# Kernel optimization log

Hardware: AMD Instinct MI355X
Metric: run time of the kernel (lower is better)

## Reference

```python
import jax, jax.numpy as jnp
import numpy as np

B, T, N = 8, 168, 1024
FD, FS, FF = 16, 32, 8
DL, DG, HE, E = 128, 128, 4, 16384
BN = B * N


def _lstm_last(x, Wih, Whh, bih, bhh):
    # x: (BN, T, FD); PyTorch gate order i, f, g, o
    h0 = jnp.zeros((x.shape[0], Whh.shape[1]), x.dtype)
    def step(carry, xt):
        h, c = carry
        g = xt @ Wih.T + h @ Whh.T + bih + bhh
        i, f, gg, o = jnp.split(g, 4, axis=-1)
        c = jax.nn.sigmoid(f) * c + jax.nn.sigmoid(i) * jnp.tanh(gg)
        h = jax.nn.sigmoid(o) * jnp.tanh(c)
        return (h, c), None
    (h, _), _ = jax.lax.scan(step, (h0, h0), jnp.swapaxes(x, 0, 1))
    return h


def _ln(x, g, b):
    mu = x.mean(-1, keepdims=True)
    v = ((x - mu) ** 2).mean(-1, keepdims=True)
    return (x - mu) / jnp.sqrt(v + 1e-5) * g + b


def _gat(x, src, dst, ea, W, a_src, a_dst, a_edge, We, bias):
    # PyG GATConv: concat=False (mean over heads), edge_dim=1, LeakyReLU(0.2)
    xl = (x @ W.T).reshape(BN, HE, -1)                 # (BN, H, C)
    as_ = jnp.sum(xl * a_src, -1)                      # (BN, H)
    ad_ = jnp.sum(xl * a_dst, -1)
    ep = (ea @ We.T).reshape(-1, HE, xl.shape[-1])     # (Eb, H, C)
    ae_ = jnp.sum(ep * a_edge, -1)                     # (Eb, H)
    alpha = jax.nn.leaky_relu(as_[src] + ad_[dst] + ae_, 0.2)
    amax = jax.ops.segment_max(alpha, dst, num_segments=BN)
    ex = jnp.exp(alpha - amax[dst])
    den = jax.ops.segment_sum(ex, dst, num_segments=BN)
    w = ex / den[dst]                                  # softmax over incoming edges
    out = jax.ops.segment_sum(w[:, :, None] * xl[src], dst, num_segments=BN)
    return out.mean(axis=1) + bias


def _forward(fl, edge_index):
    (dyn, fcst, sta, ew,
     lWih, lWhh, lbih, lbhh, sW, sb, fW, fb, uW, ub,
     g0W, g0as, g0ad, g0ae, g0We, g0b,
     g1W, g1as, g1ad, g1ae, g1We, g1b,
     n0g, n0b, n1g, n1b, oW, ob) = fl
    x = jnp.transpose(dyn, (0, 2, 1, 3)).reshape(BN, T, FD)
    z = _lstm_last(x, lWih, lWhh, lbih, lbhh)
    s = jax.nn.relu(sta.reshape(BN, -1) @ sW.T + sb)
    f = jax.nn.relu(fcst.reshape(BN, -1) @ fW.T + fb)
    h = jax.nn.relu(jnp.concatenate([z, s, f], -1) @ uW.T + ub)
    # batch the graph: B disjoint copies with node offsets
    off = (jnp.arange(B) * N)[:, None]
    src = (edge_index[0][None] + off).reshape(-1)
    dst = (edge_index[1][None] + off).reshape(-1)
    ea = jnp.tile(ew.reshape(-1, 1), (B, 1))           # (B*E, 1)
    # PyG GATConv default add_self_loops=True, fill_value='mean' of incoming edge attrs
    deg = jax.ops.segment_sum(jnp.ones_like(ea), dst, num_segments=BN)
    loop_ea = jax.ops.segment_sum(ea, dst, num_segments=BN) / jnp.maximum(deg, 1.0)
    loops = jnp.arange(BN)
    src = jnp.concatenate([src, loops])
    dst = jnp.concatenate([dst, loops])
    ea = jnp.concatenate([ea, loop_ea], 0)
    # hop 0: relu on delta (not last hop), residual (res_proj=None since DL==DG), LayerNorm
    d0 = jax.nn.relu(_gat(h, src, dst, ea, g0W, g0as, g0ad, g0ae, g0We, g0b))
    h = _ln(h + d0, n0g, n0b)
    # hop 1: last hop, no relu on delta
    d1 = _gat(h, src, dst, ea, g1W, g1as, g1ad, g1ae, g1We, g1b)
    h = _ln(h + d1, n1g, n1b)
    return (h @ oW.T + ob).reshape(B, N)


def setup_inputs():
    key = jax.random.key(0)
    ks = iter(jax.random.split(key, 48))
    def rn(shape, s=0.08):
        return jax.random.normal(next(ks), shape, jnp.float32) * s
    HO = HE * DG  # heads * out_channels
    return dict(
        dynamic_features=rn((B, T, N, FD), 1.0),
        forecast_features=rn((B, N, FF), 1.0),
        static_features=rn((B, N, FS), 1.0),
        edge_index=jax.random.randint(next(ks), (2, E), 0, N),
        edge_weight=jax.random.uniform(next(ks), (E,), jnp.float32),
        lstm_Wih=rn((4 * DL, FD)), lstm_Whh=rn((4 * DL, DL)),
        lstm_bih=rn((4 * DL,)), lstm_bhh=rn((4 * DL,)),
        static_W=rn((DL, FS)), static_b=rn((DL,)),
        fcst_W=rn((DL, FF)), fcst_b=rn((DL,)),
        fusion_W=rn((DL, 3 * DL)), fusion_b=rn((DL,)),
        gat0_W=rn((HO, DL)), gat0_att_src=rn((1, HE, DG)), gat0_att_dst=rn((1, HE, DG)),
        gat0_att_edge=rn((1, HE, DG)), gat0_We=rn((HO, 1)), gat0_bias=rn((DG,)),
        gat1_W=rn((HO, DG)), gat1_att_src=rn((1, HE, DG)), gat1_att_dst=rn((1, HE, DG)),
        gat1_att_edge=rn((1, HE, DG)), gat1_We=rn((HO, 1)), gat1_bias=rn((DG,)),
        ln0_g=jnp.ones((DG,), jnp.float32), ln0_b=jnp.zeros((DG,), jnp.float32),
        ln1_g=jnp.ones((DG,), jnp.float32), ln1_b=jnp.zeros((DG,), jnp.float32),
        out_W=rn((1, DG)), out_b=rn((1,)),
    )


def reference(dynamic_features, forecast_features, static_features, edge_weight,
              lstm_Wih, lstm_Whh, lstm_bih, lstm_bhh, static_W, static_b,
              fcst_W, fcst_b, fusion_W, fusion_b,
              gat0_W, gat0_att_src, gat0_att_dst, gat0_att_edge, gat0_We, gat0_bias,
              gat1_W, gat1_att_src, gat1_att_dst, gat1_att_edge, gat1_We, gat1_bias,
              ln0_g, ln0_b, ln1_g, ln1_b, out_W, out_b, edge_index):
    fl = (dynamic_features, forecast_features, static_features, edge_weight,
          lstm_Wih, lstm_Whh, lstm_bih, lstm_bhh, static_W, static_b,
          fcst_W, fcst_b, fusion_W, fusion_b,
          gat0_W, gat0_att_src, gat0_att_dst, gat0_att_edge, gat0_We, gat0_bias,
          gat1_W, gat1_att_src, gat1_att_dst, gat1_att_edge, gat1_We, gat1_bias,
          ln0_g, ln0_b, ln1_g, ln1_b, out_W, out_b)
    return _forward(fl, edge_index)
```

## Files before the change

### kernel.cpp

```cpp
#include <hip/hip_runtime.h>
#include <hip/hip_bf16.h>
#include <stdint.h>

#define BB 8
#define TT 168
#define NN 1024
#define BN_ 8192
#define FD_ 16
#define EE 16384

typedef short short8 __attribute__((ext_vector_type(8)));
typedef __bf16 bf16x8 __attribute__((ext_vector_type(8)));
typedef float f32x4 __attribute__((ext_vector_type(4)));

#if __has_builtin(__builtin_amdgcn_exp2f)
#define EXP2(x) __builtin_amdgcn_exp2f(x)
#else
#define EXP2(x) exp2f(x)
#endif
#if __has_builtin(__builtin_amdgcn_rcpf)
#define RCPF(x) __builtin_amdgcn_rcpf(x)
#else
#define RCPF(x) (1.f / (x))
#endif
#define L2E 1.4426950408889634f
#define T2E 2.8853900817779268f

static __device__ __forceinline__ float b2f(ushort s) {
    unsigned u = ((unsigned)s) << 16;
    return __builtin_bit_cast(float, u);
}
static __device__ __forceinline__ float b2f_lo(unsigned u) {
    return __builtin_bit_cast(float, u << 16);
}
static __device__ __forceinline__ float b2f_hi(unsigned u) {
    return __builtin_bit_cast(float, u & 0xffff0000u);
}
static __device__ __forceinline__ ushort f2b(float f) {
    unsigned u = __builtin_bit_cast(unsigned, f);
    unsigned lsb = (u >> 16) & 1u;
    u += 0x7fffu + lsb;
    return (ushort)(u >> 16);
}
static __device__ __forceinline__ ushort f2b_fast(float f) {
    unsigned u = __builtin_bit_cast(unsigned, f);
    return (ushort)((u + 0x8000u) >> 16);
}
static __device__ __forceinline__ f32x4 mfma16(short8 a, short8 b, f32x4 c) {
    return __builtin_amdgcn_mfma_f32_16x16x32_bf16(
        __builtin_bit_cast(bf16x8, a), __builtin_bit_cast(bf16x8, b), c, 0, 0, 0);
}

#define O_WIH 0
#define O_WHH 8192
#define O_STA 73728
#define O_FCS 335872
#define O_SW  401408
#define O_FW  405504
#define O_UW  406528
#define O_G0W 455680
#define O_G1W 521216
#define O_END 586752

__global__ void cast_kernel(const float* __restrict__ Wih, const float* __restrict__ Whh,
                            const float* __restrict__ sta, const float* __restrict__ fcst,
                            const float* __restrict__ sW, const float* __restrict__ fW,
                            const float* __restrict__ uW, const float* __restrict__ g0W,
                            const float* __restrict__ g1W, ushort* __restrict__ dst) {
    const int i = blockIdx.x * 256 + threadIdx.x;
    if (i >= O_END) return;
    float v;
    if      (i < O_WHH) v = Wih[i - O_WIH];
    else if (i < O_STA) v = Whh[i - O_WHH];
    else if (i < O_FCS) v = sta[i - O_STA];
    else if (i < O_SW)  v = fcst[i - O_FCS];
    else if (i < O_FW)  v = sW[i - O_SW];
    else if (i < O_UW)  v = fW[i - O_FW];
    else if (i < O_G0W) v = uW[i - O_UW];
    else if (i < O_G1W) v = g0W[i - O_G0W];
    else                v = g1W[i - O_G1W];
    dst[i] = f2b(v);
}

__global__ __launch_bounds__(1024) void prep_kernel(
    const int* __restrict__ ei, const float* __restrict__ ew,
    const float* __restrict__ We0, const float* __restrict__ ae0,
    const float* __restrict__ We1, const float* __restrict__ ae1,
    int* __restrict__ deg0, int* __restrict__ offs, float* __restrict__ loopea,
    int* __restrict__ eidx, float* __restrict__ se) {
    __shared__ int degL[1024];
    __shared__ float wsL[1024];
    __shared__ int sc[1024];
    __shared__ float seL[8];
    const int t = threadIdx.x;
    degL[t] = 0; wsL[t] = 0.f;
    if (t < 8) seL[t] = 0.f;
    __syncthreads();
    for (int e = t; e < EE; e += 1024) {
        const int d = ei[EE + e];
        atomicAdd(&degL[d], 1);
        atomicAdd(&wsL[d], ew[e]);
    }
    __syncthreads();
    const int d = degL[t];
    sc[t] = d;
    __syncthreads();
    for (int o = 1; o < 1024; o <<= 1) {
        const int v = (t >= o) ? sc[t - o] : 0;
        __syncthreads();
        sc[t] += v;
        __syncthreads();
    }
    const int excl = sc[t] - d;
    offs[t] = excl;
    deg0[t] = d;
    loopea[t] = wsL[t] / fmaxf((float)d, 1.f);
    degL[t] = excl;
    __syncthreads();
    for (int e = t; e < EE; e += 1024) {
        const int dd = ei[EE + e];
        const int slot = atomicAdd(&degL[dd], 1);
        eidx[slot] = e;
    }
    const int g = t >> 7, k = t & 127;
    const int head = g & 3;
    const float* W = (g >> 2) ? We1 : We0;
    const float* A = (g >> 2) ? ae1 : ae0;
    atomicAdd(&seL[g], W[head * 128 + k] * A[head * 128 + k]);
    __syncthreads();
    if (t < 8) se[t] = seL[t];
}

__global__ __launch_bounds__(256, 2) void lstm_kernel(
    const float* __restrict__ dyn,
    const ushort* __restrict__ Wih,
    const ushort* __restrict__ Whh,
    const float* __restrict__ bih,
    const float* __restrict__ bhh,
    ushort* __restrict__ zsf)
{
    constexpr int HS = 168;
    __shared__ ushort hbuf[2][16 * HS];

    const int tid = threadIdx.x;
    const int blk = blockIdx.x;
    const int b = blk >> 6;
    const int n0 = (blk & 63) << 4;
    const int w = tid >> 6, lane = tid & 63, quad = lane >> 4, m = lane & 15;

    short8 Bf[5][4][2];
    float ci[2], cf[2], cg[2], co[2];
#pragma unroll
    for (int jj = 0; jj < 2; jj++) {
        const int u = (2 * w + jj) * 16 + m;
#pragma unroll
        for (int g = 0; g < 4; g++) {
            const int grow = g * 128 + u;
#pragma unroll
            for (int kt = 0; kt < 4; kt++)
                Bf[kt][g][jj] = *(const short8*)(Whh + grow * 128 + kt * 32 + quad * 8);
            if (quad < 2) Bf[4][g][jj] = *(const short8*)(Wih + grow * 16 + quad * 8);
            else          Bf[4][g][jj] = short8{0, 0, 0, 0, 0, 0, 0, 0};
        }
        ci[jj] = -L2E * (bih[u] + bhh[u]);
        cf[jj] = -L2E * (bih[128 + u] + bhh[128 + u]);
        cg[jj] =  T2E * (bih[256 + u] + bhh[256 + u]);
        co[jj] = -L2E * (bih[384 + u] + bhh[384 + u]);
    }

    float c[2][4];
#pragma unroll
    for (int jj = 0; jj < 2; jj++)
#pragma unroll
        for (int r = 0; r < 4; r++) c[jj][r] = 0.f;

    for (int i = tid; i < 2 * 16 * HS; i += 256) ((ushort*)hbuf)[i] = 0;
    __syncthreads();

    const int xn = tid >> 4, xf = tid & 15;
    const size_t xbase = (size_t)b * TT * NN * FD_ + (size_t)(n0 + xn) * FD_ + xf;
    hbuf[0][xn * HS + 128 + xf] = f2b(dyn[xbase]);
    float xv = dyn[xbase + (size_t)NN * FD_];
    __syncthreads();

    for (int t = 0; t < TT; t++) {
        const ushort* rb = hbuf[t & 1];
        ushort* wb = hbuf[(t + 1) & 1];
        if (t + 1 < TT) wb[xn * HS + 128 + xf] = f2b(xv);
        if (t + 2 < TT) xv = dyn[xbase + (size_t)(t + 2) * NN * FD_];

        f32x4 acc[4][2];
#pragma unroll
        for (int g = 0; g < 4; g++)
#pragma unroll
            for (int jj = 0; jj < 2; jj++) acc[g][jj] = f32x4{0.f, 0.f, 0.f, 0.f};
#pragma unroll
        for (int kt = 0; kt < 5; kt++) {
            short8 a = *(const short8*)&rb[m * HS + kt * 32 + quad * 8];
#pragma unroll
            for (int g = 0; g < 4; g++)
#pragma unroll
                for (int jj = 0; jj < 2; jj++)
                    acc[g][jj] = mfma16(a, Bf[kt][g][jj], acc[g][jj]);
        }

#pragma unroll
        for (int jj = 0; jj < 2; jj++) {
            const int u = (2 * w + jj) * 16 + m;
#pragma unroll
            for (int r = 0; r < 4; r++) {
                const int n = quad * 4 + r;
                const float Di = 1.f + EXP2(fmaf(acc[0][jj][r], -L2E, ci[jj]));
                const float Df = 1.f + EXP2(fmaf(acc[1][jj][r], -L2E, cf[jj]));
                const float Eg = EXP2(fmaf(acc[2][jj][r], T2E, cg[jj]));
                const float Do = 1.f + EXP2(fmaf(acc[3][jj][r], -L2E, co[jj]));
                const float R  = RCPF(Di * (1.f + Eg));
                const float sf = RCPF(Df);
                const float cc = fmaf(sf, c[jj][r], (Eg - 1.f) * R);
                c[jj][r] = cc;
                const float Ec = EXP2(T2E * cc);
                const float h = (Ec - 1.f) * RCPF(Do * (1.f + Ec));
                wb[n * HS + u] = f2b_fast(h);
                if (t == TT - 1) zsf[(size_t)(blk * 16 + n) * 384 + u] = f2b_fast(h);
            }
        }
        __syncthreads();
    }
}

__global__ __launch_bounds__(256) void gemm_sf_kernel(
    const ushort* __restrict__ staB, const ushort* __restrict__ sWB,
    const float* __restrict__ sb,
    const ushort* __restrict__ fcsB, const ushort* __restrict__ fWB,
    const float* __restrict__ fb, ushort* __restrict__ zsf) {
    const int tid = threadIdx.x;
    const int lane = tid & 63, quad = lane >> 4, m = lane & 15;
    int wave = blockIdx.x * 4 + (tid >> 6);
    const short8 z8 = short8{0, 0, 0, 0, 0, 0, 0, 0};
    short8 a, bf;
    int r0, c0, ocol;
    const float* bias;
    if (wave < 4096) {
        r0 = (wave >> 3) * 16; c0 = (wave & 7) * 16; ocol = 128; bias = sb;
        a  = *(const short8*)(staB + (size_t)(r0 + m) * 32 + quad * 8);
        bf = *(const short8*)(sWB + (size_t)(c0 + m) * 32 + quad * 8);
    } else {
        wave -= 4096;
        r0 = (wave >> 3) * 16; c0 = (wave & 7) * 16; ocol = 256; bias = fb;
        a  = (quad == 0) ? *(const short8*)(fcsB + (size_t)(r0 + m) * 8) : z8;
        bf = (quad == 0) ? *(const short8*)(fWB + (size_t)(c0 + m) * 8) : z8;
    }
    f32x4 acc = mfma16(a, bf, f32x4{0.f, 0.f, 0.f, 0.f});
    const float bv = bias[c0 + m];
#pragma unroll
    for (int r = 0; r < 4; r++) {
        const int row = r0 + quad * 4 + r;
        zsf[(size_t)row * 384 + ocol + c0 + m] = f2b(fmaxf(acc[r] + bv, 0.f));
    }
}

__global__ __launch_bounds__(256) void gemm_fusion_kernel(
    const ushort* __restrict__ A, const ushort* __restrict__ Bt,
    const float* __restrict__ bias, ushort* __restrict__ hB, float* __restrict__ hF) {
    const int tid = threadIdx.x;
    const int lane = tid & 63, quad = lane >> 4, m = lane & 15;
    const int wave = blockIdx.x * 4 + (tid >> 6);
    const int r0 = (wave >> 3) * 16, c0 = (wave & 7) * 16;
    f32x4 acc = f32x4{0.f, 0.f, 0.f, 0.f};
#pragma unroll
    for (int kt = 0; kt < 12; kt++) {
        const int k = kt * 32 + quad * 8;
        short8 a  = *(const short8*)(A + (size_t)(r0 + m) * 384 + k);
        short8 bf = *(const short8*)(Bt + (size_t)(c0 + m) * 384 + k);
        acc = mfma16(a, bf, acc);
    }
    const int col = c0 + m;
    const float bv = bias[col];
#pragma unroll
    for (int r = 0; r < 4; r++) {
        const int row = r0 + quad * 4 + r;
        const float v = fmaxf(acc[r] + bv, 0.f);
        hB[(size_t)row * 128 + col] = f2b(v);
        hF[(size_t)row * 128 + col] = v;
    }
}

__global__ __launch_bounds__(256) void gemmatt_kernel(
    const ushort* __restrict__ hB, const ushort* __restrict__ W,
    const float* __restrict__ asrc, const float* __restrict__ adst,
    ushort* __restrict__ xl, float* __restrict__ as_, float* __restrict__ ad_) {
    const int tid = threadIdx.x;
    const int lane = tid & 63, quad = lane >> 4, m = lane & 15;
    const int w = tid >> 6;
    const int r0 = blockIdx.x * 16;
    f32x4 acc[8];
#pragma unroll
    for (int ct = 0; ct < 8; ct++) acc[ct] = f32x4{0.f, 0.f, 0.f, 0.f};
#pragma unroll
    for (int kt = 0; kt < 4; kt++) {
        const int k = kt * 32 + quad * 8;
        short8 a = *(const short8*)(hB + (size_t)(r0 + m) * 128 + k);
#pragma unroll
        for (int ct = 0; ct < 8; ct++) {
            short8 bf = *(const short8*)(W + (size_t)(w * 128 + ct * 16 + m) * 128 + k);
            acc[ct] = mfma16(a, bf, acc[ct]);
        }
    }
    float sa[4] = {0.f, 0.f, 0.f, 0.f}, sd[4] = {0.f, 0.f, 0.f, 0.f};
#pragma unroll
    for (int ct = 0; ct < 8; ct++) {
        const int col = w * 128 + ct * 16 + m;
        const float av = asrc[col], dv = adst[col];
#pragma unroll
        for (int r = 0; r < 4; r++) {
            const float v = acc[ct][r];
            xl[(size_t)(r0 + quad * 4 + r) * 512 + col] = f2b(v);
            sa[r] = fmaf(v, av, sa[r]);
            sd[r] = fmaf(v, dv, sd[r]);
        }
    }
#pragma unroll
    for (int o = 1; o < 16; o <<= 1) {
#pragma unroll
        for (int r = 0; r < 4; r++) {
            sa[r] += __shfl_xor(sa[r], o);
            sd[r] += __shfl_xor(sd[r], o);
        }
    }
    if (m == 0) {
#pragma unroll
        for (int r = 0; r < 4; r++) {
            const int node = r0 + quad * 4 + r;
            as_[node * 4 + w] = sa[r];
            ad_[node * 4 + w] = sd[r];
        }
    }
}

__global__ __launch_bounds__(256) void edge_exp_kernel(
    const int* __restrict__ ei, const float* __restrict__ ew,
    const float* __restrict__ as_, const float* __restrict__ ad_,
    const float* __restrict__ se4, float* __restrict__ pexp) {
    const int idx = blockIdx.x * 256 + threadIdx.x;
    const int b = idx >> 14, e = idx & (EE - 1);
    const int src = b * 1024 + ei[e];
    const int dst = b * 1024 + ei[EE + e];
    const float eaw = ew[e];
    const float4 s4 = *(const float4*)(as_ + src * 4);
    const float4 d4 = *(const float4*)(ad_ + dst * 4);
    float4 p;
    float* pp = (float*)&p;
    const float* s = (const float*)&s4;
    const float* d = (const float*)&d4;
#pragma unroll
    for (int h = 0; h < 4; h++) {
        float a = s[h] + d[h] + eaw * se4[h];
        a = (a < 0.f) ? 0.2f * a : a;
        pp[h] = EXP2(fminf(a, 60.f) * L2E);
    }
    *(float4*)(pexp + (size_t)idx * 4) = p;
}

__global__ __launch_bounds__(256) void gat_kernel(
    float* __restrict__ hF, ushort* __restrict__ hB, const ushort* __restrict__ xl,
    const float* __restrict__ as_, const float* __restrict__ ad_,
    const float* __restrict__ pexp,
    const int* __restrict__ eidx, const int* __restrict__ offs,
    const int* __restrict__ deg0, const float* __restrict__ loopea,
    const int* __restrict__ ei,
    const float* __restrict__ se4, const float* __restrict__ bias,
    const float* __restrict__ lng, const float* __restrict__ lnb, int relu,
    int writeOut, const float* __restrict__ oW, const float* __restrict__ ob,
    float* __restrict__ out) {
    const int lane = threadIdx.x & 63;
    const int c2 = lane * 2;
    const int v = blockIdx.x * 4 + (threadIdx.x >> 6);
    const int b = v >> 10, n = v & 1023;
    const int dg = deg0[n], off = offs[n];

    const float lea = loopea[n];
    const float4 s4 = *(const float4*)(as_ + v * 4);
    const float4 d4 = *(const float4*)(ad_ + v * 4);
    const float* sp = (const float*)&s4;
    const float* dp = (const float*)&d4;
    float den[4], num0[4], num1[4];
#pragma unroll
    for (int h = 0; h < 4; h++) {
        float a = sp[h] + dp[h] + lea * se4[h];
        a = (a < 0.f) ? 0.2f * a : a;
        const float p = EXP2(fminf(a, 60.f) * L2E);
        den[h] = p;
        const unsigned x01 = *(const unsigned*)(xl + (size_t)v * 512 + h * 128 + c2);
        num0[h] = p * b2f_lo(x01);
        num1[h] = p * b2f_hi(x01);
    }
    for (int i = 0; i < dg; i++) {
        const int e = eidx[off + i];
        const int src = b * 1024 + ei[e];
        const float4 p4 = *(const float4*)(pexp + (size_t)(b * EE + e) * 4);
        const float* p = (const float*)&p4;
        const ushort* xr = xl + (size_t)src * 512 + c2;
#pragma unroll
        for (int h = 0; h < 4; h++) {
            const unsigned x01 = *(const unsigned*)(xr + h * 128);
            den[h] += p[h];
            num0[h] = fmaf(p[h], b2f_lo(x01), num0[h]);
            num1[h] = fmaf(p[h], b2f_hi(x01), num1[h]);
        }
    }
    float o0 = 0.f, o1 = 0.f;
#pragma unroll
    for (int h = 0; h < 4; h++) {
        const float inv = RCPF(den[h]);
        o0 = fmaf(num0[h], inv, o0);
        o1 = fmaf(num1[h], inv, o1);
    }

    const float2 bv = *(const float2*)(bias + c2);
    float d0 = o0 * 0.25f + bv.x;
    float d1 = o1 * 0.25f + bv.y;
    if (relu) { d0 = fmaxf(d0, 0.f); d1 = fmaxf(d1, 0.f); }
    const float2 hv = *(const float2*)(hF + (size_t)v * 128 + c2);
    const float x0 = hv.x + d0;
    const float x1 = hv.y + d1;

    float s = x0 + x1;
#pragma unroll
    for (int o = 32; o; o >>= 1) s += __shfl_xor(s, o);
    const float mu = s * (1.f / 128.f);
    const float e0 = x0 - mu, e1 = x1 - mu;
    float vs = e0 * e0 + e1 * e1;
#pragma unroll
    for (int o = 32; o; o >>= 1) vs += __shfl_xor(vs, o);
    const float r = rsqrtf(vs * (1.f / 128.f) + 1e-5f);
    const float2 lg = *(const float2*)(lng + c2);
    const float2 lb = *(const float2*)(lnb + c2);
    const float y0 = e0 * r * lg.x + lb.x;
    const float y1 = e1 * r * lg.y + lb.y;
    if (writeOut) {
        const float2 ow = *(const float2*)(oW + c2);
        float t = y0 * ow.x + y1 * ow.y;
#pragma unroll
        for (int o = 32; o; o >>= 1) t += __shfl_xor(t, o);
        if (lane == 0) out[v] = t + ob[0];
    } else {
        *(float2*)(hF + (size_t)v * 128 + c2) = float2{y0, y1};
        const unsigned pk = (unsigned)f2b(y0) | ((unsigned)f2b(y1) << 16);
        *(unsigned*)(hB + (size_t)v * 128 + c2) = pk;
    }
}

extern "C" void kernel_launch(void* const* d_in, const int* in_sizes, int n_in,
                              void* d_out, int out_size, void* d_ws, size_t ws_size,
                              hipStream_t stream) {
    const float* dyn  = (const float*)d_in[0];
    const float* fcst = (const float*)d_in[1];
    const float* sta  = (const float*)d_in[2];
    const int*   ei   = (const int*)d_in[3];
    const float* ew   = (const float*)d_in[4];
    const float* lWih = (const float*)d_in[5];
    const float* lWhh = (const float*)d_in[6];
    const float* lbih = (const float*)d_in[7];
    const float* lbhh = (const float*)d_in[8];
    const float* sW = (const float*)d_in[9];
    const float* sb = (const float*)d_in[10];
    const float* fW = (const float*)d_in[11];
    const float* fb = (const float*)d_in[12];
    const float* uW = (const float*)d_in[13];
    const float* ub = (const float*)d_in[14];
    const float* g0W  = (const float*)d_in[15];
    const float* g0as = (const float*)d_in[16];
    const float* g0ad = (const float*)d_in[17];
    const float* g0ae = (const float*)d_in[18];
    const float* g0We = (const float*)d_in[19];
    const float* g0b  = (const float*)d_in[20];
    const float* g1W  = (const float*)d_in[21];
    const float* g1as = (const float*)d_in[22];
    const float* g1ad = (const float*)d_in[23];
    const float* g1ae = (const float*)d_in[24];
    const float* g1We = (const float*)d_in[25];
    const float* g1b  = (const float*)d_in[26];
    const float* ln0g = (const float*)d_in[27];
    const float* ln0b = (const float*)d_in[28];
    const float* ln1g = (const float*)d_in[29];
    const float* ln1b = (const float*)d_in[30];
    const float* oW = (const float*)d_in[31];
    const float* ob = (const float*)d_in[32];

    char* p = (char*)d_ws;
    ushort* castB = (ushort*)p; p += (size_t)O_END * 2 + 512;
    ushort* zsf = (ushort*)p;  p += (size_t)BN_ * 384 * 2;
    float*  hF  = (float*)p;   p += (size_t)BN_ * 128 * 4;
    ushort* hB  = (ushort*)p;  p += (size_t)BN_ * 128 * 2;
    ushort* xl  = (ushort*)p;  p += (size_t)BN_ * 512 * 2;
    float*  asb = (float*)p;   p += (size_t)BN_ * 4 * 4;
    float*  adb = (float*)p;   p += (size_t)BN_ * 4 * 4;
    int*    deg0   = (int*)p;   p += 4096;
    int*    offs   = (int*)p;   p += 4096;
    float*  loopea = (float*)p; p += 4096;
    int*    eidx   = (int*)p;   p += (size_t)EE * 4;
    float*  se     = (float*)p; p += 256;
    float*  pexp   = (float*)zsf;

    const ushort* WihB = castB + O_WIH;
    const ushort* WhhB = castB + O_WHH;
    const ushort* staB = castB + O_STA;
    const ushort* fcsB = castB + O_FCS;
    const ushort* sWB  = castB + O_SW;
    const ushort* fWB  = castB + O_FW;
    const ushort* uWB  = castB + O_UW;
    const ushort* g0WB = castB + O_G0W;
    const ushort* g1WB = castB + O_G1W;

    cast_kernel<<<(O_END + 255) / 256, 256, 0, stream>>>(lWih, lWhh, sta, fcst, sW, fW,
                                                         uW, g0W, g1W, castB);
    prep_kernel<<<1, 1024, 0, stream>>>(ei, ew, g0We, g0ae, g1We, g1ae,
                                        deg0, offs, loopea, eidx, se);

    lstm_kernel<<<512, 256, 0, stream>>>(dyn, WihB, WhhB, lbih, lbhh, zsf);
    gemm_sf_kernel<<<2048, 256, 0, stream>>>(staB, sWB, sb, fcsB, fWB, fb, zsf);
    gemm_fusion_kernel<<<1024, 256, 0, stream>>>(zsf, uWB, ub, hB, hF);

    gemmatt_kernel<<<512, 256, 0, stream>>>(hB, g0WB, g0as, g0ad, xl, asb, adb);
    edge_exp_kernel<<<512, 256, 0, stream>>>(ei, ew, asb, adb, se, pexp);
    gat_kernel<<<2048, 256, 0, stream>>>(hF, hB, xl, asb, adb, pexp, eidx, offs, deg0,
                                         loopea, ei, se, g0b, ln0g, ln0b, 1,
                                         0, oW, ob, (float*)d_out);
    gemmatt_kernel<<<512, 256, 0, stream>>>(hB, g1WB, g1as, g1ad, xl, asb, adb);
    edge_exp_kernel<<<512, 256, 0, stream>>>(ei, ew, asb, adb, se + 4, pexp);
    gat_kernel<<<2048, 256, 0, stream>>>(hF, hB, xl, asb, adb, pexp, eidx, offs, deg0,
                                         loopea, ei, se + 4, g1b, ln1g, ln1b, 0,
                                         1, oW, ob, (float*)d_out);
}
```

Baseline: 567.3 us.

## Fuse edge attention exp into GAT aggregation and stagger LSTM block priorities

Removes the separate edge_exp kernel and recomputes each edge's LeakyReLU/exp attention weight inline inside the GAT gather loop, dropping two launches and the pexp round trip through memory. In exchange every head computation is redone per destination wave (64 lanes redundantly), adding a gathered as_ load per edge. Separately, the LSTM kernel makes odd blocks sleep briefly at start and raises wave priority around the MFMA section, trying to desynchronize blocks so matrix and transcendental phases interleave across waves.

```diff
diff --git a/kernel.cpp b/kernel.cpp
--- a/kernel.cpp
+++ b/kernel.cpp
@@ -183,6 +183,10 @@
     float xv = dyn[xbase + (size_t)NN * FD_];
     __syncthreads();
 
+#if __has_builtin(__builtin_amdgcn_s_sleep)
+    if (blk & 1) __builtin_amdgcn_s_sleep(33);
+#endif
+
     for (int t = 0; t < TT; t++) {
         const ushort* rb = hbuf[t & 1];
         ushort* wb = hbuf[(t + 1) & 1];
@@ -194,6 +198,9 @@
         for (int g = 0; g < 4; g++)
 #pragma unroll
             for (int jj = 0; jj < 2; jj++) acc[g][jj] = f32x4{0.f, 0.f, 0.f, 0.f};
+#if __has_builtin(__builtin_amdgcn_s_setprio)
+        __builtin_amdgcn_s_setprio(1);
+#endif
 #pragma unroll
         for (int kt = 0; kt < 5; kt++) {
             short8 a = *(const short8*)&rb[m * HS + kt * 32 + quad * 8];
@@ -203,6 +210,9 @@
                 for (int jj = 0; jj < 2; jj++)
                     acc[g][jj] = mfma16(a, Bf[kt][g][jj], acc[g][jj]);
         }
+#if __has_builtin(__builtin_amdgcn_s_setprio)
+        __builtin_amdgcn_s_setprio(0);
+#endif
 
 #pragma unroll
         for (int jj = 0; jj < 2; jj++) {
@@ -337,37 +347,12 @@
     }
 }
 
-__global__ __launch_bounds__(256) void edge_exp_kernel(
-    const int* __restrict__ ei, const float* __restrict__ ew,
-    const float* __restrict__ as_, const float* __restrict__ ad_,
-    const float* __restrict__ se4, float* __restrict__ pexp) {
-    const int idx = blockIdx.x * 256 + threadIdx.x;
-    const int b = idx >> 14, e = idx & (EE - 1);
-    const int src = b * 1024 + ei[e];
-    const int dst = b * 1024 + ei[EE + e];
-    const float eaw = ew[e];
-    const float4 s4 = *(const float4*)(as_ + src * 4);
-    const float4 d4 = *(const float4*)(ad_ + dst * 4);
-    float4 p;
-    float* pp = (float*)&p;
-    const float* s = (const float*)&s4;
-    const float* d = (const float*)&d4;
-#pragma unroll
-    for (int h = 0; h < 4; h++) {
-        float a = s[h] + d[h] + eaw * se4[h];
-        a = (a < 0.f) ? 0.2f * a : a;
-        pp[h] = EXP2(fminf(a, 60.f) * L2E);
-    }
-    *(float4*)(pexp + (size_t)idx * 4) = p;
-}
-
 __global__ __launch_bounds__(256) void gat_kernel(
     float* __restrict__ hF, ushort* __restrict__ hB, const ushort* __restrict__ xl,
     const float* __restrict__ as_, const float* __restrict__ ad_,
-    const float* __restrict__ pexp,
     const int* __restrict__ eidx, const int* __restrict__ offs,
     const int* __restrict__ deg0, const float* __restrict__ loopea,
-    const int* __restrict__ ei,
+    const int* __restrict__ ei, const float* __restrict__ ew,
     const float* __restrict__ se4, const float* __restrict__ bias,
     const float* __restrict__ lng, const float* __restrict__ lnb, int relu,
     int writeOut, const float* __restrict__ oW, const float* __restrict__ ob,
@@ -378,15 +363,18 @@
     const int b = v >> 10, n = v & 1023;
     const int dg = deg0[n], off = offs[n];
 
+    const float se0 = se4[0], se1 = se4[1], se2 = se4[2], se3 = se4[3];
+    const float4 d4 = *(const float4*)(ad_ + v * 4);
+    const float* dp = (const float*)&d4;
+
     const float lea = loopea[n];
     const float4 s4 = *(const float4*)(as_ + v * 4);
-    const float4 d4 = *(const float4*)(ad_ + v * 4);
     const float* sp = (const float*)&s4;
-    const float* dp = (const float*)&d4;
     float den[4], num0[4], num1[4];
+    const float sev[4] = {se0, se1, se2, se3};
 #pragma unroll
     for (int h = 0; h < 4; h++) {
-        float a = sp[h] + dp[h] + lea * se4[h];
+        float a = sp[h] + dp[h] + lea * sev[h];
         a = (a < 0.f) ? 0.2f * a : a;
         const float p = EXP2(fminf(a, 60.f) * L2E);
         den[h] = p;
@@ -397,15 +385,19 @@
     for (int i = 0; i < dg; i++) {
         const int e = eidx[off + i];
         const int src = b * 1024 + ei[e];
-        const float4 p4 = *(const float4*)(pexp + (size_t)(b * EE + e) * 4);
-        const float* p = (const float*)&p4;
+        const float eaw = ew[e];
+        const float4 se_ = *(const float4*)(as_ + src * 4);
+        const float* sp_ = (const float*)&se_;
         const ushort* xr = xl + (size_t)src * 512 + c2;
 #pragma unroll
         for (int h = 0; h < 4; h++) {
+            float a = sp_[h] + dp[h] + eaw * sev[h];
+            a = (a < 0.f) ? 0.2f * a : a;
+            const float p = EXP2(fminf(a, 60.f) * L2E);
             const unsigned x01 = *(const unsigned*)(xr + h * 128);
-            den[h] += p[h];
-            num0[h] = fmaf(p[h], b2f_lo(x01), num0[h]);
-            num1[h] = fmaf(p[h], b2f_hi(x01), num1[h]);
+            den[h] += p;
+            num0[h] = fmaf(p, b2f_lo(x01), num0[h]);
+            num1[h] = fmaf(p, b2f_hi(x01), num1[h]);
         }
     }
     float o0 = 0.f, o1 = 0.f;
@@ -500,7 +492,6 @@
     float*  loopea = (float*)p; p += 4096;
     int*    eidx   = (int*)p;   p += (size_t)EE * 4;
     float*  se     = (float*)p; p += 256;
-    float*  pexp   = (float*)zsf;
 
     const ushort* WihB = castB + O_WIH;
     const ushort* WhhB = castB + O_WHH;
@@ -522,13 +513,11 @@
     gemm_fusion_kernel<<<1024, 256, 0, stream>>>(zsf, uWB, ub, hB, hF);
 
     gemmatt_kernel<<<512, 256, 0, stream>>>(hB, g0WB, g0as, g0ad, xl, asb, adb);
-    edge_exp_kernel<<<512, 256, 0, stream>>>(ei, ew, asb, adb, se, pexp);
-    gat_kernel<<<2048, 256, 0, stream>>>(hF, hB, xl, asb, adb, pexp, eidx, offs, deg0,
-                                         loopea, ei, se, g0b, ln0g, ln0b, 1,
+    gat_kernel<<<2048, 256, 0, stream>>>(hF, hB, xl, asb, adb, eidx, offs, deg0,
+                                         loopea, ei, ew, se, g0b, ln0g, ln0b, 1,
                                          0, oW, ob, (float*)d_out);
     gemmatt_kernel<<<512, 256, 0, stream>>>(hB, g1WB, g1as, g1ad, xl, asb, adb);
-    edge_exp_kernel<<<512, 256, 0, stream>>>(ei, ew, asb, adb, se + 4, pexp);
-    gat_kernel<<<2048, 256, 0, stream>>>(hF, hB, xl, asb, adb, pexp, eidx, offs, deg0,
-                                         loopea, ei, se + 4, g1b, ln1g, ln1b, 0,
+    gat_kernel<<<2048, 256, 0, stream>>>(hF, hB, xl, asb, adb, eidx, offs, deg0,
+                                         loopea, ei, ew, se + 4, g1b, ln1g, ln1b, 0,
                                          1, oW, ob, (float*)d_out);
 }
```

New measurement: 579.5 us. +2.2%, slower.
